# Performance work log

Hardware: AMD Instinct MI355X
Metric: run time of the kernel (lower is better)

## Reference

```python
import jax, jax.numpy as jnp
import numpy as np

V, C, L, H, N = 32000, 1024, 2, 16, 64
B, T, FF = 2, 1024, 4096
DW, DA, DV, DG = 64, 64, 32, 128


def setup_inputs() -> dict:
    ks = iter(jax.random.split(jax.random.key(0), 64))
    def nrm(shape, s=0.02):
        return jax.random.normal(next(ks), shape, jnp.float32) * s
    def uni(shape):
        return jax.random.uniform(next(ks), shape, jnp.float32)
    return dict(
        idx=jax.random.randint(next(ks), (B, T), 0, V, dtype=jnp.int32),
        emb_w=nrm((V, C)),
        ln0_g=jnp.ones((C,), jnp.float32), ln0_b=jnp.zeros((C,), jnp.float32),
        ln1_g=jnp.ones((L, C), jnp.float32), ln1_b=jnp.zeros((L, C), jnp.float32),
        ln2_g=jnp.ones((L, C), jnp.float32), ln2_b=jnp.zeros((L, C), jnp.float32),
        lnx_g=jnp.ones((L, C), jnp.float32), lnx_b=jnp.zeros((L, C), jnp.float32),
        lnout_g=jnp.ones((C,), jnp.float32), lnout_b=jnp.zeros((C,), jnp.float32),
        x_mix=uni((L, 6, C)),
        w0=nrm((L, C), 0.3) - 0.5,
        w1=nrm((L, C, DW)), w2=nrm((L, DW, C), 0.1),
        a0=jnp.zeros((L, C), jnp.float32), a1=nrm((L, C, DA)), a2=nrm((L, DA, C), 0.1),
        v0=jnp.ones((L, C), jnp.float32), v1=nrm((L, C, DV)), v2=nrm((L, DV, C), 0.1),
        g1=nrm((L, C, DG)), g2=nrm((L, DG, C), 0.1),
        k_k=jnp.full((L, C), 0.85, jnp.float32),
        k_a=jnp.ones((L, C), jnp.float32),
        r_k=nrm((L, H, N), 0.1),
        Wr=nrm((L, C, C)), Wk=nrm((L, C, C)), Wv=nrm((L, C, C)), Wo=nrm((L, C, C)),
        ffn_xk=uni((L, C)),
        ffn_k=nrm((L, C, FF)), ffn_v=nrm((L, FF, C)),
        time_state=nrm((L, H, N, N), 0.1),
        head_w=nrm((C, V)),
    )


def _ln(x, g, b, eps=1e-5):
    m = jnp.mean(x, -1, keepdims=True)
    v = jnp.mean(jnp.square(x - m), -1, keepdims=True)
    return (x - m) * jax.lax.rsqrt(v + eps) * g + b


def _shift(x):  # time_shift: prepend zero token, drop last
    return jnp.pad(x, ((0, 0), (1, 0), (0, 0)))[:, :-1]


def _rwkv7_scan(r, k, v, w, a, b, S0):
    # r,k,v,w,a,b: (B,T,H,N); S0: (B,H,N,N) laid out [value_dim, key_dim]
    # S_t = S_{t-1} * diag(exp(w_t)) + S_{t-1} a_t b_t^T + v_t k_t^T ; y_t = S_t r_t
    def step(S, inp):
        r_, k_, v_, w_, a_, b_ = inp
        sa = jnp.einsum('bhij,bhj->bhi', S, a_)
        S = (S * jnp.exp(w_)[:, :, None, :]
             + sa[..., None] * b_[:, :, None, :]
             + v_[..., None] * k_[:, :, None, :])
        y = jnp.einsum('bhij,bhj->bhi', S, r_)
        return S, y
    xs = tuple(jnp.moveaxis(t, 1, 0) for t in (r, k, v, w, a, b))
    S, ys = jax.lax.scan(step, S0, xs)
    return jnp.moveaxis(ys, 0, 1), S  # (B,T,H,N), (B,H,N,N)


def _forward(idx, emb_w, ln0_g, ln0_b, ln1_g, ln1_b, ln2_g, ln2_b, lnx_g, lnx_b,
             lnout_g, lnout_b, x_mix, w0, w1, w2, a0, a1, a2, v0, v1, v2,
             g1, g2, k_k, k_a, r_k, Wr, Wk, Wv, Wo, ffn_xk, ffn_k, ffn_v,
             time_state, head_w):
    Bv, Tv = idx.shape
    Lh, Hh, Nh = r_k.shape
    x = emb_w[idx]                      # (B,T,C)
    v_first = jnp.zeros_like(x)
    for i in range(Lh):
        if i == 0:
            x = _ln(x, ln0_g, ln0_b)
        xin = _ln(x, ln1_g[i], ln1_b[i])
        xx = _shift(xin) - xin
        xr, xw, xk, xv, xa_, xg = (xin + xx * x_mix[i, j] for j in range(6))
        r = xr @ Wr[i]
        w = -jax.nn.softplus(-(w0[i] + jnp.tanh(xw @ w1[i]) @ w2[i])) - 0.5
        k = xk @ Wk[i]
        v = xv @ Wv[i]
        if i == 0:
            v_first = v
        else:
            v = v + (v_first - v) * jax.nn.sigmoid(v0[i] + (xv @ v1[i]) @ v2[i])
        a = jax.nn.sigmoid(a0[i] + (xa_ @ a1[i]) @ a2[i])
        g = jax.nn.sigmoid(xg @ g1[i]) @ g2[i]
        kk = (k * k_k[i]).reshape(Bv, Tv, Hh, Nh)
        kk = kk / jnp.maximum(jnp.linalg.norm(kk, axis=-1, keepdims=True), 1e-12)
        kk = kk.reshape(Bv, Tv, -1)
        k2 = k * (1.0 + (a - 1.0) * k_a[i])
        rs = lambda t: t.reshape(Bv, Tv, Hh, Nh)
        S0 = jnp.broadcast_to(time_state[i], (Bv, Hh, Nh, Nh))
        y, _S = _rwkv7_scan(rs(r), rs(k2), rs(v), rs(w), rs(-kk), rs(kk * a), S0)
        # ln_x = GroupNorm(H, C, eps=64e-5): per-head normalization
        m = y.mean(-1, keepdims=True)
        var = jnp.square(y - m).mean(-1, keepdims=True)
        y = (y - m) * jax.lax.rsqrt(var + 64e-5)
        y = y * lnx_g[i].reshape(Hh, Nh) + lnx_b[i].reshape(Hh, Nh)
        bonus = (rs(r) * rs(k2) * r_k[i]).sum(-1, keepdims=True) * rs(v)
        y = (y + bonus).reshape(Bv, Tv, -1)
        x = x + (y * g) @ Wo[i]
        # channel mix (x070 FFN)
        xc = _ln(x, ln2_g[i], ln2_b[i])
        kx = xc + (_shift(xc) - xc) * ffn_xk[i]
        x = x + jnp.square(jax.nn.relu(kx @ ffn_k[i])) @ ffn_v[i]
    return _ln(x, lnout_g, lnout_b) @ head_w


def reference(idx, emb_w, ln0_g, ln0_b, ln1_g, ln1_b, ln2_g, ln2_b, lnx_g, lnx_b,
              lnout_g, lnout_b, x_mix, w0, w1, w2, a0, a1, a2, v0, v1, v2,
              g1, g2, k_k, k_a, r_k, Wr, Wk, Wv, Wo, ffn_xk, ffn_k, ffn_v,
              time_state, head_w):
    return _forward(idx, emb_w, ln0_g, ln0_b, ln1_g, ln1_b, ln2_g, ln2_b,
                    lnx_g, lnx_b, lnout_g, lnout_b, x_mix, w0, w1, w2,
                    a0, a1, a2, v0, v1, v2, g1, g2, k_k, k_a, r_k,
                    Wr, Wk, Wv, Wo, ffn_xk, ffn_k, ffn_v, time_state, head_w)
```

## Files before the change

kernel.cpp:

```cpp
#include <hip/hip_runtime.h>
#include <hip/hip_bf16.h>
#include <math.h>

#define V_  32000
#define C_  1024
#define L_  2
#define H_  16
#define N_  64
#define B_  2
#define T_  1024
#define FF_ 4096
#define DW_ 64
#define DA_ 64
#define DV_ 32
#define DG_ 128
#define BT_  (B_*T_)
#define BTC_ (BT_*C_)

typedef float floatx4 __attribute__((ext_vector_type(4)));
typedef short shortx8 __attribute__((ext_vector_type(8)));
typedef __attribute__((address_space(1))) unsigned int gu32;
typedef __attribute__((address_space(3))) unsigned int su32;

__device__ __forceinline__ float sigf(float x){ return 1.0f/(1.0f+expf(-x)); }
__device__ __forceinline__ unsigned short f2bf(float x){
  __hip_bfloat16 h = __float2bfloat16(x);
  return *(unsigned short*)&h;
}
__device__ __forceinline__ void gload16(const void* g, void* l){
  __builtin_amdgcn_global_load_lds((const gu32*)g, (su32*)l, 16, 0, 0);
}

__device__ __forceinline__ float dpp_red16(float s){
  s += __int_as_float(__builtin_amdgcn_update_dpp(0, __float_as_int(s), 0xB1, 0xf, 0xf, true));
  s += __int_as_float(__builtin_amdgcn_update_dpp(0, __float_as_int(s), 0x4E, 0xf, 0xf, true));
  s += __int_as_float(__builtin_amdgcn_update_dpp(0, __float_as_int(s), 0x141, 0xf, 0xf, true));
  s += __int_as_float(__builtin_amdgcn_update_dpp(0, __float_as_int(s), 0x140, 0xf, 0xf, true));
  return s;
}

__global__ void k_embed(const int* __restrict__ idx, const float* __restrict__ emb,
                        float* __restrict__ x){
  int i = blockIdx.x*256 + threadIdx.x;
  if (i >= BTC_) return;
  int row = i / C_, c = i - row*C_;
  x[i] = emb[(size_t)idx[row]*C_ + c];
}

__global__ void k_ln(const float* __restrict__ x, const float* __restrict__ g,
                     const float* __restrict__ b, float* __restrict__ out){
  int row = blockIdx.x;
  const float* xr = x + (size_t)row*C_;
  float s = 0.f, s2 = 0.f;
  for (int c = threadIdx.x; c < C_; c += 256){ float v = xr[c]; s += v; s2 += v*v; }
  for (int o = 32; o > 0; o >>= 1){ s += __shfl_xor(s,o); s2 += __shfl_xor(s2,o); }
  __shared__ float w1s[4], w2s[4];
  int wid = threadIdx.x >> 6, lane = threadIdx.x & 63;
  if (lane == 0){ w1s[wid] = s; w2s[wid] = s2; }
  __syncthreads();
  if (threadIdx.x == 0){
    float a = 0.f, bb = 0.f;
    for (int i = 0; i < 4; i++){ a += w1s[i]; bb += w2s[i]; }
    w1s[0] = a; w2s[0] = bb;
  }
  __syncthreads();
  float mean = w1s[0] * (1.0f/C_);
  float var  = w2s[0] * (1.0f/C_) - mean*mean;
  float r = rsqrtf(var + 1e-5f);
  float* orow = out + (size_t)row*C_;
  for (int c = threadIdx.x; c < C_; c += 256)
    orow[c] = (xr[c]-mean)*r*g[c] + b[c];
}

__global__ void k_mix6(const float* __restrict__ xin, const float* __restrict__ mixl,
                       unsigned short* __restrict__ m6){
  int i = blockIdx.x*256 + threadIdx.x;
  if (i >= BTC_) return;
  int bt = i / C_, c = i - bt*C_;
  int t = bt % T_;
  float cur = xin[i];
  float prev = (t > 0) ? xin[i - C_] : 0.f;
  float d = prev - cur;
#pragma unroll
  for (int j = 0; j < 6; j++)
    m6[(size_t)j*BTC_ + i] = f2bf(cur + d*mixl[j*C_ + c]);
}

__global__ void k_ffnmix(const float* __restrict__ xc, const float* __restrict__ fxk,
                         unsigned short* __restrict__ kx){
  int i = blockIdx.x*256 + threadIdx.x;
  if (i >= BTC_) return;
  int bt = i / C_, c = i - bt*C_;
  int t = bt % T_;
  float cur = xc[i];
  float prev = (t > 0) ? xc[i - C_] : 0.f;
  kx[i] = f2bf(cur + (prev - cur)*fxk[c]);
}

__global__ void k_cast16(const float* __restrict__ in, unsigned short* __restrict__ out){
  int i = blockIdx.x*256 + threadIdx.x;
  if (i >= BTC_) return;
  out[i] = f2bf(in[i]);
}

__global__ void k_decay(const float* __restrict__ w0, float* __restrict__ wd){
  int i = blockIdx.x*256 + threadIdx.x;
  if (i >= BTC_) return;
  int c = i % C_;
  wd[i] = sigf(w0[c] + wd[i]) * 0.60653065971263342f;
}

__global__ void k_asig(const float* __restrict__ a0, float* __restrict__ a){
  int i = blockIdx.x*256 + threadIdx.x;
  if (i >= BTC_) return;
  int c = i % C_;
  a[i] = sigf(a0[c] + a[i]);
}

__global__ void k_vmix(const float* __restrict__ v0, const float* __restrict__ vv,
                       const float* __restrict__ vf, float* __restrict__ v){
  int i = blockIdx.x*256 + threadIdx.x;
  if (i >= BTC_) return;
  int c = i % C_;
  float s = sigf(v0[c] + vv[i]);
  v[i] = v[i] + (vf[i] - v[i])*s;
}

__global__ void k_kk(const float* __restrict__ kkw, const float* __restrict__ kaw,
                     const float* __restrict__ a, float* __restrict__ k,
                     float* __restrict__ kk, float* __restrict__ bba){
  int bth = blockIdx.x;
  int lane = threadIdx.x;
  int bt = bth / H_, h = bth - bt*H_;
  int cix = h*N_ + lane;
  size_t gi = (size_t)bt*C_ + cix;
  float kv = k[gi];
  float kkv = kv * kkw[cix];
  float ss = kkv*kkv;
  for (int o = 32; o > 0; o >>= 1) ss += __shfl_xor(ss,o);
  float nrm = fmaxf(sqrtf(ss), 1e-12f);
  float kkn = kkv / nrm;
  kk[gi] = kkn;
  float av = a[gi];
  bba[gi] = -kkn*av;
  k[gi] = kv * (1.f + (av - 1.f)*kaw[cix]);
}

#define SCHUNK 8
__global__ __launch_bounds__(256) void k_scan(
    const float* __restrict__ r, const float* __restrict__ k2,
    const float* __restrict__ v, const float* __restrict__ wd,
    const float* __restrict__ kk, const float* __restrict__ bba,
    const float* __restrict__ S0, float* __restrict__ y){
  int bh = blockIdx.x;
  int b = bh / H_, h = bh - b*H_;
  int tid = threadIdx.x;
  int wave = tid >> 6, lane = tid & 63;
  int rg = tid >> 4;
  int cg = tid & 15;
  int r0 = rg*4, c0 = cg*4;

  __shared__ __attribute__((aligned(16))) float buf[2][6][SCHUNK][64];

  float S[4][4];
#pragma unroll
  for (int ri = 0; ri < 4; ri++){
    const floatx4 s0 = *(const floatx4*)&S0[((size_t)h*N_ + r0 + ri)*N_ + c0];
#pragma unroll
    for (int ci = 0; ci < 4; ci++) S[ri][ci] = s0[ci];
  }

  size_t hoff = ((size_t)b*T_)*C_ + (size_t)h*N_;

  auto do_stage = [&](int t0, int bi){
#pragma unroll
    for (int q = 0; q < 3; q++){
      int u = wave*3 + q;
      int vec = u >> 1, tt4 = (u & 1)*4;
      int tt = tt4 + (lane >> 4);
      const float* src;
      switch (vec){
        case 0: src = r;   break;
        case 1: src = k2;  break;
        case 2: src = v;   break;
        case 3: src = wd;  break;
        case 4: src = kk;  break;
        default: src = bba; break;
      }
      src += hoff + (size_t)(t0 + tt)*C_ + (size_t)((lane & 15)*4);
      gload16(src, &buf[bi][vec][tt4][0]);
    }
  };

  do_stage(0, 0);
  asm volatile("s_waitcnt vmcnt(0)" ::: "memory");
  __syncthreads();

  const int NC = T_/SCHUNK;
  for (int c = 0; c < NC; c++){
    int bi = c & 1;
    if (c + 1 < NC) do_stage((c+1)*SCHUNK, bi ^ 1);
    size_t off = hoff + (size_t)(c*SCHUNK)*C_;
#pragma unroll
    for (int tt = 0; tt < SCHUNK; tt++, off += C_){
      const floatx4 rv  = *(const floatx4*)&buf[bi][0][tt][c0];
      const floatx4 kv  = *(const floatx4*)&buf[bi][1][tt][c0];
      const floatx4 vv  = *(const floatx4*)&buf[bi][2][tt][r0];
      const floatx4 dd  = *(const floatx4*)&buf[bi][3][tt][c0];
      const floatx4 kkv = *(const floatx4*)&buf[bi][4][tt][c0];
      const floatx4 bav = *(const floatx4*)&buf[bi][5][tt][c0];
      float sa[4];
#pragma unroll
      for (int ri = 0; ri < 4; ri++){
        float s = S[ri][0]*kkv[0];
        s = fmaf(S[ri][1], kkv[1], s);
        s = fmaf(S[ri][2], kkv[2], s);
        s = fmaf(S[ri][3], kkv[3], s);
        sa[ri] = dpp_red16(s);
      }
      float yv[4];
#pragma unroll
      for (int ri = 0; ri < 4; ri++){
        float vi = vv[ri];
        float yy = 0.f;
#pragma unroll
        for (int ci = 0; ci < 4; ci++){
          float t0v = fmaf(vi, kv[ci], sa[ri]*bav[ci]);
          float s = fmaf(S[ri][ci], dd[ci], t0v);
          S[ri][ci] = s;
          yy = fmaf(s, rv[ci], yy);
        }
        yv[ri] = dpp_red16(yy);
      }
      if (cg == 0){
        floatx4 o; o[0]=yv[0]; o[1]=yv[1]; o[2]=yv[2]; o[3]=yv[3];
        *(floatx4*)&y[off + r0] = o;
      }
    }
    asm volatile("s_waitcnt vmcnt(0)" ::: "memory");
    __syncthreads();
  }
}

__global__ void k_gnb(const float* __restrict__ lxg, const float* __restrict__ lxb,
                      const float* __restrict__ rk, const float* __restrict__ r,
                      const float* __restrict__ k2, const float* __restrict__ v,
                      const float* __restrict__ g, const float* __restrict__ y,
                      unsigned short* __restrict__ yg){
  int bth = blockIdx.x;
  int lane = threadIdx.x;
  int bt = bth / H_, h = bth - bt*H_;
  int cix = h*N_ + lane;
  size_t gi = (size_t)bt*C_ + cix;
  float yv = y[gi];
  float s = yv;
  for (int o = 32; o > 0; o >>= 1) s += __shfl_xor(s,o);
  float mean = s * (1.0f/N_);
  float d = yv - mean;
  float s2 = d*d;
  for (int o = 32; o > 0; o >>= 1) s2 += __shfl_xor(s2,o);
  float var = s2 * (1.0f/N_);
  float yn = d * rsqrtf(var + 64e-5f) * lxg[cix] + lxb[cix];
  float dv = r[gi]*k2[gi]*rk[h*N_ + lane];
  for (int o = 32; o > 0; o >>= 1) dv += __shfl_xor(dv,o);
  yg[gi] = f2bf((yn + dv*v[gi]) * g[gi]);
}

__global__ void k_tc(const float* __restrict__ in, unsigned short* __restrict__ out,
                     int R, int Cc, int Cpad){
  __shared__ float t[32][33];
  int c0 = blockIdx.x*32, r0 = blockIdx.y*32;
  int tx = threadIdx.x, ty = threadIdx.y;
  for (int i = ty; i < 32; i += 8){
    int r = r0+i, c = c0+tx;
    t[i][tx] = (r < R && c < Cc) ? in[(size_t)r*Cc + c] : 0.f;
  }
  __syncthreads();
  for (int i = ty; i < 32; i += 8){
    int oc = c0+i, orr = r0+tx;
    if (oc < Cpad && orr < R) out[(size_t)oc*R + orr] = f2bf(t[tx][i]);
  }
}

__global__ __launch_bounds__(256) void k_mgemm(
    const short* __restrict__ A, int lda, const short* __restrict__ Bt,
    float* __restrict__ Cf, unsigned short* __restrict__ Cb, int ldc,
    int K, int ep){
  __shared__ __attribute__((aligned(16))) short As[128*32];
  __shared__ __attribute__((aligned(16))) short Bs[128*32];
  int m0 = blockIdx.y*128, n0 = blockIdx.x*128;
  int tid = threadIdx.x, wave = tid >> 6, lane = tid & 63;
  int lhi = lane >> 4, llo = lane & 15;
  int wm = wave & 1, wn = wave >> 1;
  int arow = lane >> 2, acol = (lane & 3)*8;
  floatx4 acc[4][4];
#pragma unroll
  for (int i = 0; i < 4; i++)
#pragma unroll
    for (int j = 0; j < 4; j++) acc[i][j] = (floatx4){0.f,0.f,0.f,0.f};

  for (int k0 = 0; k0 < K; k0 += 32){
#pragma unroll
    for (int q = 0; q < 2; q++){
      int r0 = wave*32 + q*16;
      gload16(A  + (size_t)(m0 + r0 + arow)*lda + k0 + acol, As + r0*32);
      gload16(Bt + (size_t)(n0 + r0 + arow)*K   + k0 + acol, Bs + r0*32);
    }
    __syncthreads();
    shortx8 af[4], bfv[4];
#pragma unroll
    for (int mi = 0; mi < 4; mi++)
      af[mi] = *(const shortx8*)(As + ((wm*64 + mi*16 + llo)*32 + lhi*8));
#pragma unroll
    for (int nj = 0; nj < 4; nj++)
      bfv[nj] = *(const shortx8*)(Bs + ((wn*64 + nj*16 + llo)*32 + lhi*8));
#pragma unroll
    for (int mi = 0; mi < 4; mi++)
#pragma unroll
      for (int nj = 0; nj < 4; nj++)
        acc[mi][nj] = __builtin_amdgcn_mfma_f32_16x16x32_bf16(af[mi], bfv[nj], acc[mi][nj], 0, 0, 0);
    __syncthreads();
  }
#pragma unroll
  for (int mi = 0; mi < 4; mi++){
#pragma unroll
    for (int nj = 0; nj < 4; nj++){
      int gr0 = m0 + wm*64 + mi*16 + lhi*4;
      int gc  = n0 + wn*64 + nj*16 + llo;
#pragma unroll
      for (int rg = 0; rg < 4; rg++){
        size_t ci = (size_t)(gr0 + rg)*ldc + gc;
        float v = acc[mi][nj][rg];
        switch (ep){
          case 0: Cf[ci] = v; break;
          case 1: Cf[ci] += v; break;
          case 2: Cb[ci] = f2bf(v); break;
          case 3: Cb[ci] = f2bf(tanhf(v)); break;
          case 4: Cb[ci] = f2bf(sigf(v)); break;
          case 5: { float rr = fmaxf(v, 0.f); Cb[ci] = f2bf(rr*rr); } break;
        }
      }
    }
  }
}

extern "C" void kernel_launch(void* const* d_in, const int* in_sizes, int n_in,
                              void* d_out, int out_size, void* d_ws, size_t ws_size,
                              hipStream_t stream){
  const int*   idx     = (const int*)  d_in[0];
  const float* emb_w   = (const float*)d_in[1];
  const float* ln0_g   = (const float*)d_in[2];
  const float* ln0_b   = (const float*)d_in[3];
  const float* ln1_g   = (const float*)d_in[4];
  const float* ln1_b   = (const float*)d_in[5];
  const float* ln2_g   = (const float*)d_in[6];
  const float* ln2_b   = (const float*)d_in[7];
  const float* lnx_g   = (const float*)d_in[8];
  const float* lnx_b   = (const float*)d_in[9];
  const float* lnout_g = (const float*)d_in[10];
  const float* lnout_b = (const float*)d_in[11];
  const float* x_mix   = (const float*)d_in[12];
  const float* w0      = (const float*)d_in[13];
  const float* w1      = (const float*)d_in[14];
  const float* w2      = (const float*)d_in[15];
  const float* a0      = (const float*)d_in[16];
  const float* a1      = (const float*)d_in[17];
  const float* a2      = (const float*)d_in[18];
  const float* v0      = (const float*)d_in[19];
  const float* v1      = (const float*)d_in[20];
  const float* v2      = (const float*)d_in[21];
  const float* g1      = (const float*)d_in[22];
  const float* g2      = (const float*)d_in[23];
  const float* k_k     = (const float*)d_in[24];
  const float* k_a     = (const float*)d_in[25];
  const float* r_k     = (const float*)d_in[26];
  const float* Wr      = (const float*)d_in[27];
  const float* Wk      = (const float*)d_in[28];
  const float* Wv      = (const float*)d_in[29];
  const float* Wo      = (const float*)d_in[30];
  const float* ffn_xk  = (const float*)d_in[31];
  const float* ffn_k   = (const float*)d_in[32];
  const float* ffn_v   = (const float*)d_in[33];
  const float* tstate  = (const float*)d_in[34];
  const float* head_w  = (const float*)d_in[35];
  float* out = (float*)d_out;

  char* p = (char*)d_ws;
  auto alloc = [&](size_t bytes)->void*{ void* r = (void*)p; p += (bytes + 255) & ~(size_t)255; return r; };
  float* x      = (float*)alloc((size_t)BTC_*4);
  float* vfirst = (float*)alloc((size_t)BTC_*4);
  float* xin    = (float*)alloc((size_t)BTC_*4);
  float* rb     = (float*)alloc((size_t)BTC_*4);
  float* wdec   = (float*)alloc((size_t)BTC_*4);
  float* kb     = (float*)alloc((size_t)BTC_*4);
  float* vb     = (float*)alloc((size_t)BTC_*4);
  float* ab     = (float*)alloc((size_t)BTC_*4);
  float* kkb    = (float*)alloc((size_t)BTC_*4);
  float* yb     = (float*)alloc((size_t)BTC_*4);
  float* gb     = (float*)alloc((size_t)BTC_*4);
  unsigned short* act16 = (unsigned short*)alloc((size_t)6*BTC_*2);
  unsigned short* m_r = act16;
  unsigned short* m_w = act16 + 1*(size_t)BTC_;
  unsigned short* m_k = act16 + 2*(size_t)BTC_;
  unsigned short* m_v = act16 + 3*(size_t)BTC_;
  unsigned short* m_a = act16 + 4*(size_t)BTC_;
  unsigned short* m_g = act16 + 5*(size_t)BTC_;
  unsigned short* yg16  = m_r;
  unsigned short* kx16  = m_w;
  unsigned short* hid16 = m_k;
  unsigned short* xh16  = m_r;
  unsigned short* w16 = (unsigned short*)alloc((size_t)BT_*128*2);
  unsigned short* a16 = (unsigned short*)alloc((size_t)BT_*128*2);
  unsigned short* v16 = (unsigned short*)alloc((size_t)BT_*128*2);
  unsigned short* g16 = (unsigned short*)alloc((size_t)BT_*128*2);
  unsigned short *WrT[L_], *WkT[L_], *WvT[L_], *WoT[L_];
  unsigned short *w1T[L_], *a1T[L_], *v1T[L_], *g1T[L_];
  unsigned short *w2T[L_], *a2T[L_], *v2T[L_], *g2T[L_];
  unsigned short *fkT[L_], *fvT[L_];
  for (int l = 0; l < L_; l++){
    WrT[l] = (unsigned short*)alloc((size_t)C_*C_*2);
    WkT[l] = (unsigned short*)alloc((size_t)C_*C_*2);
    WvT[l] = (unsigned short*)alloc((size_t)C_*C_*2);
    WoT[l] = (unsigned short*)alloc((size_t)C_*C_*2);
    w1T[l] = (unsigned short*)alloc((size_t)128*C_*2);
    a1T[l] = (unsigned short*)alloc((size_t)128*C_*2);
    v1T[l] = (unsigned short*)alloc((size_t)128*C_*2);
    g1T[l] = (unsigned short*)alloc((size_t)128*C_*2);
    w2T[l] = (unsigned short*)alloc((size_t)C_*64*2);
    a2T[l] = (unsigned short*)alloc((size_t)C_*64*2);
    v2T[l] = (unsigned short*)alloc((size_t)C_*32*2);
    g2T[l] = (unsigned short*)alloc((size_t)C_*128*2);
    fkT[l] = (unsigned short*)alloc((size_t)FF_*C_*2);
    fvT[l] = (unsigned short*)alloc((size_t)C_*FF_*2);
  }
  unsigned short* hwT = (unsigned short*)alloc((size_t)V_*C_*2);

  dim3 blk(256);
  dim3 tcb(32, 8);
  int ewg = (BTC_ + 255)/256;

  auto MG = [&](const unsigned short* A, int lda, const unsigned short* Bt,
                float* Cf, unsigned short* Cb, int ldc, int M, int Nn, int K, int ep){
    k_mgemm<<<dim3(Nn/128, M/128), 256, 0, stream>>>(
      (const short*)A, lda, (const short*)Bt, Cf, Cb, ldc, K, ep);
  };

  for (int l = 0; l < L_; l++){
    k_tc<<<dim3(32,32), tcb, 0, stream>>>(Wr + (size_t)l*C_*C_, WrT[l], C_, C_, C_);
    k_tc<<<dim3(32,32), tcb, 0, stream>>>(Wk + (size_t)l*C_*C_, WkT[l], C_, C_, C_);
    k_tc<<<dim3(32,32), tcb, 0, stream>>>(Wv + (size_t)l*C_*C_, WvT[l], C_, C_, C_);
    k_tc<<<dim3(32,32), tcb, 0, stream>>>(Wo + (size_t)l*C_*C_, WoT[l], C_, C_, C_);
    k_tc<<<dim3(4,32),  tcb, 0, stream>>>(w1 + (size_t)l*C_*DW_, w1T[l], C_, DW_, 128);
    k_tc<<<dim3(4,32),  tcb, 0, stream>>>(a1 + (size_t)l*C_*DA_, a1T[l], C_, DA_, 128);
    k_tc<<<dim3(4,32),  tcb, 0, stream>>>(v1 + (size_t)l*C_*DV_, v1T[l], C_, DV_, 128);
    k_tc<<<dim3(4,32),  tcb, 0, stream>>>(g1 + (size_t)l*C_*DG_, g1T[l], C_, DG_, 128);
    k_tc<<<dim3(32,2),  tcb, 0, stream>>>(w2 + (size_t)l*DW_*C_, w2T[l], DW_, C_, C_);
    k_tc<<<dim3(32,2),  tcb, 0, stream>>>(a2 + (size_t)l*DA_*C_, a2T[l], DA_, C_, C_);
    k_tc<<<dim3(32,1),  tcb, 0, stream>>>(v2 + (size_t)l*DV_*C_, v2T[l], DV_, C_, C_);
    k_tc<<<dim3(32,4),  tcb, 0, stream>>>(g2 + (size_t)l*DG_*C_, g2T[l], DG_, C_, C_);
    k_tc<<<dim3(128,32),tcb, 0, stream>>>(ffn_k + (size_t)l*C_*FF_, fkT[l], C_, FF_, FF_);
    k_tc<<<dim3(32,128),tcb, 0, stream>>>(ffn_v + (size_t)l*FF_*C_, fvT[l], FF_, C_, C_);
  }
  k_tc<<<dim3(1000,32), tcb, 0, stream>>>(head_w, hwT, C_, V_, V_);

  k_embed<<<ewg, blk, 0, stream>>>(idx, emb_w, x);

  for (int l = 0; l < L_; l++){
    const float* mixl = x_mix + ((size_t)l*6)*C_;
    if (l == 0)
      k_ln<<<BT_, blk, 0, stream>>>(x, ln0_g, ln0_b, x);
    k_ln<<<BT_, blk, 0, stream>>>(x, ln1_g + l*C_, ln1_b + l*C_, xin);
    k_mix6<<<ewg, blk, 0, stream>>>(xin, mixl, act16);

    MG(m_r, C_, WrT[l], rb, 0, C_, BT_, C_, C_, 0);
    MG(m_w, C_, w1T[l], 0, w16, 128, BT_, 128, C_, 3);
    MG(m_k, C_, WkT[l], kb, 0, C_, BT_, C_, C_, 0);
    MG(m_v, C_, WvT[l], vb, 0, C_, BT_, C_, C_, 0);
    if (l > 0)
      MG(m_v, C_, v1T[l], 0, v16, 128, BT_, 128, C_, 2);
    MG(m_a, C_, a1T[l], 0, a16, 128, BT_, 128, C_, 2);
    MG(m_g, C_, g1T[l], 0, g16, 128, BT_, 128, C_, 4);

    MG(w16, 128, w2T[l], wdec, 0, C_, BT_, C_, DW_, 0);
    k_decay<<<ewg, blk, 0, stream>>>(w0 + l*C_, wdec);
    MG(a16, 128, a2T[l], ab, 0, C_, BT_, C_, DA_, 0);
    k_asig<<<ewg, blk, 0, stream>>>(a0 + l*C_, ab);
    if (l == 0){
      hipMemcpyAsync(vfirst, vb, (size_t)BTC_*4, hipMemcpyDeviceToDevice, stream);
    } else {
      MG(v16, 128, v2T[l], xin, 0, C_, BT_, C_, DV_, 0);
      k_vmix<<<ewg, blk, 0, stream>>>(v0 + l*C_, xin, vfirst, vb);
    }
    MG(g16, 128, g2T[l], gb, 0, C_, BT_, C_, DG_, 0);

    k_kk<<<BT_*H_, 64, 0, stream>>>(k_k + l*C_, k_a + l*C_, ab, kb, kkb, xin);

    k_scan<<<B_*H_, 256, 0, stream>>>(rb, kb, vb, wdec, kkb, xin,
                                      tstate + (size_t)l*H_*N_*N_, yb);

    k_gnb<<<BT_*H_, 64, 0, stream>>>(lnx_g + l*C_, lnx_b + l*C_, r_k + (size_t)l*H_*N_,
                                     rb, kb, vb, gb, yb, yg16);

    MG(yg16, C_, WoT[l], x, 0, C_, BT_, C_, C_, 1);

    k_ln<<<BT_, blk, 0, stream>>>(x, ln2_g + l*C_, ln2_b + l*C_, xin);
    k_ffnmix<<<ewg, blk, 0, stream>>>(xin, ffn_xk + l*C_, kx16);
    MG(kx16, C_, fkT[l], 0, hid16, FF_, BT_, FF_, C_, 5);
    MG(hid16, FF_, fvT[l], x, 0, C_, BT_, C_, FF_, 1);
  }

  k_ln<<<BT_, blk, 0, stream>>>(x, lnout_g, lnout_b, xin);
  k_cast16<<<ewg, blk, 0, stream>>>(xin, xh16);
  MG(xh16, C_, hwT, out, 0, V_, BT_, V_, C_, 0);
}
```

Before: 2.601 ms.

## Split RWKV7 scan state rows across more blocks to raise parallelism

The recurrent scan kernel now splits each head's 64-row state across 8 blocks of 128 threads, with each thread holding one row segment of 4 columns instead of a 4x4 tile. This raises the grid from 32 to 256 blocks so more compute units work on the serial time loop, and it shortens each thread's per-step dependency chain. In exchange, every block redundantly loads the full r/k/w/kk/bba chunk for its head, which multiplies global and LDS traffic by 8, and each row now needs its own 16-lane reductions.

```diff
diff --git a/kernel.cpp b/kernel.cpp
--- a/kernel.cpp
+++ b/kernel.cpp
@@ -147,35 +147,37 @@
 }
 
 #define SCHUNK 8
-__global__ __launch_bounds__(256) void k_scan(
+#define SROWS  8
+__global__ __launch_bounds__(128) void k_scan(
     const float* __restrict__ r, const float* __restrict__ k2,
     const float* __restrict__ v, const float* __restrict__ wd,
     const float* __restrict__ kk, const float* __restrict__ bba,
     const float* __restrict__ S0, float* __restrict__ y){
-  int bh = blockIdx.x;
+  int bh = blockIdx.x & 31;
+  int rblk = blockIdx.x >> 5;
   int b = bh / H_, h = bh - b*H_;
   int tid = threadIdx.x;
   int wave = tid >> 6, lane = tid & 63;
   int rg = tid >> 4;
+  int row = rblk*SROWS + rg;
   int cg = tid & 15;
-  int r0 = rg*4, c0 = cg*4;
+  int c0 = cg*4;
 
   __shared__ __attribute__((aligned(16))) float buf[2][6][SCHUNK][64];
 
-  float S[4][4];
-#pragma unroll
-  for (int ri = 0; ri < 4; ri++){
-    const floatx4 s0 = *(const floatx4*)&S0[((size_t)h*N_ + r0 + ri)*N_ + c0];
-#pragma unroll
-    for (int ci = 0; ci < 4; ci++) S[ri][ci] = s0[ci];
+  float S[4];
+  {
+    const floatx4 s0 = *(const floatx4*)&S0[((size_t)h*N_ + row)*N_ + c0];
+#pragma unroll
+    for (int ci = 0; ci < 4; ci++) S[ci] = s0[ci];
   }
 
   size_t hoff = ((size_t)b*T_)*C_ + (size_t)h*N_;
 
   auto do_stage = [&](int t0, int bi){
 #pragma unroll
-    for (int q = 0; q < 3; q++){
-      int u = wave*3 + q;
+    for (int q = 0; q < 6; q++){
+      int u = wave*6 + q;
       int vec = u >> 1, tt4 = (u & 1)*4;
       int tt = tt4 + (lane >> 4);
       const float* src;
@@ -205,37 +207,25 @@
     for (int tt = 0; tt < SCHUNK; tt++, off += C_){
       const floatx4 rv  = *(const floatx4*)&buf[bi][0][tt][c0];
       const floatx4 kv  = *(const floatx4*)&buf[bi][1][tt][c0];
-      const floatx4 vv  = *(const floatx4*)&buf[bi][2][tt][r0];
+      const float   vi  = buf[bi][2][tt][row];
       const floatx4 dd  = *(const floatx4*)&buf[bi][3][tt][c0];
       const floatx4 kkv = *(const floatx4*)&buf[bi][4][tt][c0];
       const floatx4 bav = *(const floatx4*)&buf[bi][5][tt][c0];
-      float sa[4];
-#pragma unroll
-      for (int ri = 0; ri < 4; ri++){
-        float s = S[ri][0]*kkv[0];
-        s = fmaf(S[ri][1], kkv[1], s);
-        s = fmaf(S[ri][2], kkv[2], s);
-        s = fmaf(S[ri][3], kkv[3], s);
-        sa[ri] = dpp_red16(s);
+      float s = S[0]*kkv[0];
+      s = fmaf(S[1], kkv[1], s);
+      s = fmaf(S[2], kkv[2], s);
+      s = fmaf(S[3], kkv[3], s);
+      float sa = dpp_red16(s);
+      float yy = 0.f;
+#pragma unroll
+      for (int ci = 0; ci < 4; ci++){
+        float t0v = fmaf(vi, kv[ci], sa*bav[ci]);
+        float sn = fmaf(S[ci], dd[ci], t0v);
+        S[ci] = sn;
+        yy = fmaf(sn, rv[ci], yy);
       }
-      float yv[4];
-#pragma unroll
-      for (int ri = 0; ri < 4; ri++){
-        float vi = vv[ri];
-        float yy = 0.f;
-#pragma unroll
-        for (int ci = 0; ci < 4; ci++){
-          float t0v = fmaf(vi, kv[ci], sa[ri]*bav[ci]);
-          float s = fmaf(S[ri][ci], dd[ci], t0v);
-          S[ri][ci] = s;
-          yy = fmaf(s, rv[ci], yy);
-        }
-        yv[ri] = dpp_red16(yy);
-      }
-      if (cg == 0){
-        floatx4 o; o[0]=yv[0]; o[1]=yv[1]; o[2]=yv[2]; o[3]=yv[3];
-        *(floatx4*)&y[off + r0] = o;
-      }
+      float yv = dpp_red16(yy);
+      if (cg == 0) y[off + row] = yv;
     }
     asm volatile("s_waitcnt vmcnt(0)" ::: "memory");
     __syncthreads();
@@ -495,7 +485,7 @@
 
     k_kk<<<BT_*H_, 64, 0, stream>>>(k_k + l*C_, k_a + l*C_, ab, kb, kkb, xin);
 
-    k_scan<<<B_*H_, 256, 0, stream>>>(rb, kb, vb, wdec, kkb, xin,
+    k_scan<<<B_*H_*(N_/SROWS), 128, 0, stream>>>(rb, kb, vb, wdec, kkb, xin,
                                       tstate + (size_t)l*H_*N_*N_, yb);
 
     k_gnb<<<BT_*H_, 64, 0, stream>>>(lnx_g + l*C_, lnx_b + l*C_, r_k + (size_t)l*H_*N_,
```

Result: faster. 2.384 ms (-8.4%).
